# Optimization experiments

Hardware: AMD Instinct MI355X
Metric: run time of the kernel (lower is better)

## Reference

```python
import jax, jax.numpy as jnp
import numpy as np

B, T, E, H, D = 2, 2048, 1024, 16, 64
SCALE = 1.0 / float(np.sqrt(D))


def setup_inputs() -> dict:
    key = jax.random.key(0)
    ks = jax.random.split(key, 8)
    n = lambda k, sh, s=1.0: jax.random.normal(k, sh, dtype=jnp.float32) * s
    # torch nn.Linear weights are [out_features, in_features]; xavier-ish scale
    return {
        "query": n(ks[0], (B, T, E)),
        "key_": n(ks[1], (B, T, E)),
        "value": n(ks[2], (B, T, E)),
        "attn_mask": n(ks[3], (T, T), 0.1),
        "Wq": n(ks[4], (H * D, E), 1.0 / float(np.sqrt(E))),
        "Wk": n(ks[5], (H * D, E), 1.0 / float(np.sqrt(E))),
        "Wv": n(ks[6], (H * D, E), 1.0 / float(np.sqrt(E))),
        "Wo": n(ks[7], (E, H * D), 1.0 / float(np.sqrt(H * D))),
    }


def reference(query, key_, value, attn_mask, Wq, Wk, Wv, Wo):
    # projections (no bias), reshape to [B, T, H, D]
    Q = (query @ Wq.T).reshape(B, T, H, D)
    K = (key_ @ Wk.T).reshape(B, -1, H, D)
    V = (value @ Wv.T).reshape(B, -1, H, D)
    # scores [B, T, H, S]; additive [T, S] mask broadcast over B and H
    score = jnp.einsum("bthd,bshd->bths", Q, K) * SCALE
    score = score + attn_mask[:, None, :]
    prob = jax.nn.softmax(score, axis=-1)  # dropout is identity in eval mode
    attn = jnp.einsum("bths,bshd->bthd", prob, V)  # [B, T, H, D]
    x = attn.reshape(B, T, H * D) @ Wo.T  # output projection
    return x
```

## Files before the change

kernel.cpp:

```cpp
#include <hip/hip_runtime.h>


typedef __attribute__((ext_vector_type(8))) short s8v;
typedef __attribute__((ext_vector_type(4))) float f4v;

typedef __attribute__((address_space(1))) const void* gas_t;
typedef __attribute__((address_space(3))) void* las_t;

#define GLOAD_LDS(src, dst) \
  __builtin_amdgcn_global_load_lds((gas_t)(src), (las_t)(dst), 16, 0, 0)
#define MFMA16(a, b, c) __builtin_amdgcn_mfma_f32_16x16x32_bf16((a), (b), (c), 0, 0, 0)

#if __has_builtin(__builtin_amdgcn_exp2f)
#define EXP2(x) __builtin_amdgcn_exp2f(x)
#else
#define EXP2(x) exp2f(x)
#endif

static constexpr int Bn = 2, Tn = 2048, En = 1024, Hn = 16, Dn = 64;
static constexpr float kScale = 0.125f;
static constexpr float kLog2e = 1.4426950408889634f;

union P8 { s8v v; unsigned short u[8]; };

__device__ __forceinline__ unsigned short f2bf(float f) {
  unsigned int x = __float_as_uint(f);
  x += 0x7fffu + ((x >> 16) & 1u);
  return (unsigned short)(x >> 16);
}

__device__ __forceinline__ int cvtpk(float lo, float hi) {
  int r;
  asm("v_cvt_pk_bf16_f32 %0, %1, %2" : "=v"(r) : "v"(lo), "v"(hi));
  return r;
}

__device__ __forceinline__ void cast8(const float* __restrict__ src, int j,
                                      unsigned short* __restrict__ out, int i) {
  float4 a = ((const float4*)src)[2 * j];
  float4 b = ((const float4*)src)[2 * j + 1];
  P8 p;
  p.u[0] = f2bf(a.x); p.u[1] = f2bf(a.y); p.u[2] = f2bf(a.z); p.u[3] = f2bf(a.w);
  p.u[4] = f2bf(b.x); p.u[5] = f2bf(b.y); p.u[6] = f2bf(b.z); p.u[7] = f2bf(b.w);
  ((s8v*)out)[i] = p.v;
}

__global__ void cast3_kernel(const float* __restrict__ a, const float* __restrict__ b,
                             const float* __restrict__ c,
                             unsigned short* __restrict__ out, int n8) {
  int i = blockIdx.x * blockDim.x + threadIdx.x;
  const int stride = gridDim.x * blockDim.x;
  const int total = 3 * n8;
  for (; i < total; i += stride) {
    const float* src = (i < n8) ? a : (i < 2 * n8) ? b : c;
    const int j = (i < n8) ? i : (i < 2 * n8) ? i - n8 : i - 2 * n8;
    cast8(src, j, out, i);
  }
}

__global__ void cast4_kernel(const float* __restrict__ a, const float* __restrict__ b,
                             const float* __restrict__ c, const float* __restrict__ d,
                             unsigned short* __restrict__ out, int n8) {
  int i = blockIdx.x * blockDim.x + threadIdx.x;
  const int stride = gridDim.x * blockDim.x;
  const int total = 4 * n8;
  for (; i < total; i += stride) {
    const int which = i / n8;
    const float* src = (which == 0) ? a : (which == 1) ? b : (which == 2) ? c : d;
    cast8(src, i - which * n8, out, i);
  }
}

__global__ __launch_bounds__(64) void maskpack_kernel(const float* __restrict__ mask,
                                                      unsigned int* __restrict__ mPB) {
  __shared__ float tile[16][65];
  const int qt = blockIdx.x, st = blockIdx.y;
  const int tid = threadIdx.x;
#pragma unroll
  for (int i = 0; i < 16; ++i)
    tile[i][tid] = mask[(size_t)(qt * 16 + i) * Tn + st * 64 + tid];
  __syncthreads();
  const int lr = tid & 15, lg = tid >> 4;
  float o[16];
#pragma unroll
  for (int n = 0; n < 4; ++n)
#pragma unroll
    for (int rg = 0; rg < 4; ++rg)
      o[n * 4 + rg] = tile[lr][n * 16 + lg * 4 + rg] * kLog2e;
  unsigned int wds[8];
#pragma unroll
  for (int i = 0; i < 8; ++i)
    wds[i] = ((unsigned int)f2bf(o[2 * i + 1]) << 16) | f2bf(o[2 * i]);
  uint4* dst = (uint4*)(mPB + ((size_t)(qt * 32 + st) * 64 + tid) * 8);
  dst[0] = make_uint4(wds[0], wds[1], wds[2], wds[3]);
  dst[1] = make_uint4(wds[4], wds[5], wds[6], wds[7]);
}

__global__ __launch_bounds__(256) void gemm3_kernel(
    const unsigned short* __restrict__ qx, const unsigned short* __restrict__ kx,
    const unsigned short* __restrict__ vxa, const unsigned short* __restrict__ wqx,
    const unsigned short* __restrict__ wkx, const unsigned short* __restrict__ wvx,
    unsigned short* __restrict__ Qh, unsigned short* __restrict__ Kh,
    unsigned short* __restrict__ Vtg) {
  constexpr int K = 1024;
  __shared__ unsigned short As[128 * 64];
  __shared__ unsigned short Bs[128 * 64];
  const int tid = threadIdx.x;
  const int w = tid >> 6, l = tid & 63;
  const int wr = w >> 1, wc = w & 1;
  const int lr = l & 15, lg = l >> 4;

  const int id0 = blockIdx.x;
  const int rid = (id0 & 7) * 96 + (id0 >> 3);
  const int z = rid >> 8;
  const int t8 = rid & 255;
  const int m0 = (z < 2) ? (t8 >> 3) * 128 : (t8 & 7) * 128;
  const int n0 = (z < 2) ? (t8 & 7) * 128 : (t8 >> 3) * 128;

  const unsigned short* A = (z == 0) ? qx : (z == 1) ? kx : wvx;
  const unsigned short* W = (z == 0) ? wqx : (z == 1) ? wkx : vxa;

  f4v acc[4][4] = {};

  for (int k0 = 0; k0 < K; k0 += 64) {
#pragma unroll
    for (int jj = 0; jj < 4; ++jj) {
      const int q = jj * 256 + tid;
      const int r = q >> 3, c = q & 7;
      const int cs = c ^ (r & 7);
      GLOAD_LDS(A + (size_t)(m0 + r) * K + k0 + cs * 8,
                (char*)As + (jj * 256 + w * 64) * 16);
      GLOAD_LDS(W + (size_t)(n0 + r) * K + k0 + cs * 8,
                (char*)Bs + (jj * 256 + w * 64) * 16);
    }
    __syncthreads();
#pragma unroll
    for (int kk = 0; kk < 2; ++kk) {
      s8v af[4], bf[4];
      const int kc = kk * 4 + lg;
#pragma unroll
      for (int i = 0; i < 4; ++i) {
        const int ra = wr * 64 + i * 16 + lr;
        const int rb = wc * 64 + i * 16 + lr;
        af[i] = *(const s8v*)((const char*)As + ra * 128 + ((kc ^ (ra & 7)) << 4));
        bf[i] = *(const s8v*)((const char*)Bs + rb * 128 + ((kc ^ (rb & 7)) << 4));
      }
#pragma unroll
      for (int mi = 0; mi < 4; ++mi)
#pragma unroll
        for (int nj = 0; nj < 4; ++nj)
          acc[mi][nj] = MFMA16(af[mi], bf[nj], acc[mi][nj]);
    }
    __syncthreads();
  }

  const float scale = (z == 0) ? kScale * kLog2e : 1.0f;
#pragma unroll
  for (int mi = 0; mi < 4; ++mi)
#pragma unroll
    for (int nj = 0; nj < 4; ++nj)
#pragma unroll
      for (int rg = 0; rg < 4; ++rg) {
        const int row = m0 + wr * 64 + mi * 16 + lg * 4 + rg;
        const int col = n0 + wc * 64 + nj * 16 + lr;
        const float v = acc[mi][nj][rg];
        if (z < 2) {
          const int b = row >> 11, t = row & (Tn - 1);
          const int hh = col >> 6, d = col & 63;
          unsigned short* o = (z == 0) ? Qh : Kh;
          o[(((size_t)(b * Hn + hh) * Tn + t) << 6) + d] = f2bf(v * scale);
        } else {
          const int hh = row >> 6, d = row & 63;
          const int b = col >> 11, t = col & (Tn - 1);
          Vtg[((size_t)(b * Hn + hh) * 64 + d) * Tn + t] = f2bf(v);
        }
      }
}

__global__ __launch_bounds__(256) void gemm_out(const unsigned short* __restrict__ A,
                                                const unsigned short* __restrict__ W,
                                                float* __restrict__ Cout) {
  constexpr int N = 1024, K = 1024;
  __shared__ unsigned short As[2][128 * 64];
  __shared__ unsigned short Bs[2][128 * 64];
  const int tid = threadIdx.x;
  const int w = tid >> 6, l = tid & 63;
  const int wr = w >> 1, wc = w & 1;
  const int lr = l & 15, lg = l >> 4;

  const int gx = gridDim.x;
  int id = blockIdx.y * gx + blockIdx.x;
  id = (id & 7) * 32 + (id >> 3);
  const int m0 = (id / gx) * 128, n0 = (id % gx) * 128;

  auto stage = [&](int k0, int buf) {
#pragma unroll
    for (int jj = 0; jj < 4; ++jj) {
      const int q = jj * 256 + tid;
      const int r = q >> 3, c = q & 7;
      const int cs = c ^ (r & 7);
      GLOAD_LDS(A + (size_t)(m0 + r) * K + k0 + cs * 8,
                (char*)As[buf] + (jj * 256 + w * 64) * 16);
      GLOAD_LDS(W + (size_t)(n0 + r) * K + k0 + cs * 8,
                (char*)Bs[buf] + (jj * 256 + w * 64) * 16);
    }
  };

  stage(0, 0);
  __syncthreads();

  f4v acc[4][4] = {};

  for (int k0 = 0, t = 0; k0 < K; k0 += 64, ++t) {
    const int cur = t & 1;
    if (k0 + 64 < K) stage(k0 + 64, cur ^ 1);
#pragma unroll
    for (int kk = 0; kk < 2; ++kk) {
      s8v af[4], bf[4];
      const int kc = kk * 4 + lg;
#pragma unroll
      for (int i = 0; i < 4; ++i) {
        const int ra = wr * 64 + i * 16 + lr;
        const int rb = wc * 64 + i * 16 + lr;
        af[i] = *(const s8v*)((const char*)As[cur] + ra * 128 + ((kc ^ (ra & 7)) << 4));
        bf[i] = *(const s8v*)((const char*)Bs[cur] + rb * 128 + ((kc ^ (rb & 7)) << 4));
      }
#pragma unroll
      for (int mi = 0; mi < 4; ++mi)
#pragma unroll
        for (int nj = 0; nj < 4; ++nj)
          acc[mi][nj] = MFMA16(af[mi], bf[nj], acc[mi][nj]);
    }
    __syncthreads();
  }

#pragma unroll
  for (int mi = 0; mi < 4; ++mi)
#pragma unroll
    for (int nj = 0; nj < 4; ++nj)
#pragma unroll
      for (int rg = 0; rg < 4; ++rg) {
        const int row = m0 + wr * 64 + mi * 16 + lg * 4 + rg;
        const int col = n0 + wc * 64 + nj * 16 + lr;
        Cout[(size_t)row * N + col] = acc[mi][nj][rg];
      }
}

__global__ __launch_bounds__(128, 2) void attn_kernel(
    const unsigned short* __restrict__ Q,
    const unsigned short* __restrict__ Kg,
    const unsigned short* __restrict__ Vt,
    const unsigned int* __restrict__ mPB,
    unsigned short* __restrict__ Out) {
  __shared__ unsigned short Ks[2][64 * 64];
  __shared__ unsigned short Vs[2][64 * 64];

  const int tid = threadIdx.x;
  const int w = tid >> 6, lane = tid & 63;
  const int lr = lane & 15, lg = lane >> 4;

  const int lin = blockIdx.x;
  const int xcd = lin & 7, slot = lin >> 3;
  const int bh = xcd * 4 + (slot >> 5);
  const int qtB = slot & 31;
  const int b = bh >> 4, h = bh & 15;

  const size_t hoff = (size_t)bh * Tn * Dn;
  const unsigned short* Qh = Q + hoff;
  const unsigned short* Kh = Kg + hoff;
  const unsigned short* Vh = Vt + hoff;
  const int qwA = qtB * 64 + w * 32;
  const int qwB = qwA + 16;
  const unsigned int* mp = mPB + ((size_t)(qtB * 4 + w * 2) * 2048 + lane) * 8;

  auto stage = [&](int s0, int buf) {
#pragma unroll
    for (int jj = 0; jj < 4; ++jj) {
      const int cq = jj * 128 + tid;
      const int r = cq >> 3, cc = cq & 7;
      const int cs = cc ^ (r & 7);
      GLOAD_LDS(Kh + (size_t)(s0 + r) * 64 + cs * 8,
                (char*)Ks[buf] + (jj * 128 + w * 64) * 16);
      GLOAD_LDS(Vh + (size_t)r * Tn + s0 + cs * 8,
                (char*)Vs[buf] + (jj * 128 + w * 64) * 16);
    }
  };

  s8v qfA[2], qfB[2];
#pragma unroll
  for (int kk = 0; kk < 2; ++kk) {
    qfA[kk] = *(const s8v*)(Qh + (size_t)(qwA + lr) * 64 + kk * 32 + lg * 8);
    qfB[kk] = *(const s8v*)(Qh + (size_t)(qwB + lr) * 64 + kk * 32 + lg * 8);
  }

  float lsumA = 0.f, lsumB = 0.f;
  f4v oaccA[4] = {}, oaccB[4] = {};

  const int srcA = lr + ((lg & 1) << 5);
  const int srcB = srcA + 16;
  const int hi = lg >> 1;

  stage(0, 0);
  __syncthreads();

  for (int s0 = 0, t = 0; s0 < Tn; s0 += 64, ++t, mp += 512) {
    const int cur = t & 1;
    if (s0 + 64 < Tn) stage(s0 + 64, cur ^ 1);

    s8v kf[2][4], vf[2][4];
#pragma unroll
    for (int kk = 0; kk < 2; ++kk)
#pragma unroll
      for (int n = 0; n < 4; ++n) {
        const int row = n * 16 + lr;
        const int coff = ((kk * 4 + lg) ^ (lr & 7)) << 4;
        kf[kk][n] = *(const s8v*)((const char*)Ks[cur] + row * 128 + coff);
        vf[kk][n] = *(const s8v*)((const char*)Vs[cur] + row * 128 + coff);
      }

    {
      const uint4 u0 = *(const uint4*)(mp);
      const uint4 u1 = *(const uint4*)(mp + 4);
      const unsigned int wd[8] = {u0.x, u0.y, u0.z, u0.w, u1.x, u1.y, u1.z, u1.w};
      f4v scT[4];
#pragma unroll
      for (int n = 0; n < 4; ++n) {
        scT[n][0] = __uint_as_float(wd[2 * n] << 16);
        scT[n][1] = __uint_as_float(wd[2 * n] & 0xffff0000u);
        scT[n][2] = __uint_as_float(wd[2 * n + 1] << 16);
        scT[n][3] = __uint_as_float(wd[2 * n + 1] & 0xffff0000u);
      }
#pragma unroll
      for (int kk = 0; kk < 2; ++kk)
#pragma unroll
        for (int n = 0; n < 4; ++n)
          scT[n] = MFMA16(kf[kk][n], qfA[kk], scT[n]);
      float ssum = 0.f;
#pragma unroll
      for (int n = 0; n < 4; ++n)
#pragma unroll
        for (int rg = 0; rg < 4; ++rg) {
          const float p = EXP2(scT[n][rg]);
          scT[n][rg] = p;
          ssum += p;
        }
      ssum += __shfl_xor(ssum, 16);
      ssum += __shfl_xor(ssum, 32);
      lsumA += ssum;
      int pw0[4], pw1[4];
#pragma unroll
      for (int n = 0; n < 4; ++n) {
        pw0[n] = cvtpk(scT[n][0], scT[n][1]);
        pw1[n] = cvtpk(scT[n][2], scT[n][3]);
      }
#pragma unroll
      for (int kk = 0; kk < 2; ++kk) {
        const int a0 = __shfl(pw0[2 * kk], srcA), b0 = __shfl(pw0[2 * kk + 1], srcA);
        const int a1 = __shfl(pw1[2 * kk], srcA), b1 = __shfl(pw1[2 * kk + 1], srcA);
        const int a2 = __shfl(pw0[2 * kk], srcB), b2 = __shfl(pw0[2 * kk + 1], srcB);
        const int a3 = __shfl(pw1[2 * kk], srcB), b3 = __shfl(pw1[2 * kk + 1], srcB);
        union { s8v v; int x[4]; } pf;
        pf.x[0] = hi ? b0 : a0;
        pf.x[1] = hi ? b1 : a1;
        pf.x[2] = hi ? b2 : a2;
        pf.x[3] = hi ? b3 : a3;
#pragma unroll
        for (int n = 0; n < 4; ++n)
          oaccA[n] = MFMA16(pf.v, vf[kk][n], oaccA[n]);
      }
    }

    {
      const uint4 u0 = *(const uint4*)(mp + 16384);
      const uint4 u1 = *(const uint4*)(mp + 16388);
      const unsigned int wd[8] = {u0.x, u0.y, u0.z, u0.w, u1.x, u1.y, u1.z, u1.w};
      f4v scT[4];
#pragma unroll
      for (int n = 0; n < 4; ++n) {
        scT[n][0] = __uint_as_float(wd[2 * n] << 16);
        scT[n][1] = __uint_as_float(wd[2 * n] & 0xffff0000u);
        scT[n][2] = __uint_as_float(wd[2 * n + 1] << 16);
        scT[n][3] = __uint_as_float(wd[2 * n + 1] & 0xffff0000u);
      }
#pragma unroll
      for (int kk = 0; kk < 2; ++kk)
#pragma unroll
        for (int n = 0; n < 4; ++n)
          scT[n] = MFMA16(kf[kk][n], qfB[kk], scT[n]);
      float ssum = 0.f;
#pragma unroll
      for (int n = 0; n < 4; ++n)
#pragma unroll
        for (int rg = 0; rg < 4; ++rg) {
          const float p = EXP2(scT[n][rg]);
          scT[n][rg] = p;
          ssum += p;
        }
      ssum += __shfl_xor(ssum, 16);
      ssum += __shfl_xor(ssum, 32);
      lsumB += ssum;
      int pw0[4], pw1[4];
#pragma unroll
      for (int n = 0; n < 4; ++n) {
        pw0[n] = cvtpk(scT[n][0], scT[n][1]);
        pw1[n] = cvtpk(scT[n][2], scT[n][3]);
      }
#pragma unroll
      for (int kk = 0; kk < 2; ++kk) {
        const int a0 = __shfl(pw0[2 * kk], srcA), b0 = __shfl(pw0[2 * kk + 1], srcA);
        const int a1 = __shfl(pw1[2 * kk], srcA), b1 = __shfl(pw1[2 * kk + 1], srcA);
        const int a2 = __shfl(pw0[2 * kk], srcB), b2 = __shfl(pw0[2 * kk + 1], srcB);
        const int a3 = __shfl(pw1[2 * kk], srcB), b3 = __shfl(pw1[2 * kk + 1], srcB);
        union { s8v v; int x[4]; } pf;
        pf.x[0] = hi ? b0 : a0;
        pf.x[1] = hi ? b1 : a1;
        pf.x[2] = hi ? b2 : a2;
        pf.x[3] = hi ? b3 : a3;
#pragma unroll
        for (int n = 0; n < 4; ++n)
          oaccB[n] = MFMA16(pf.v, vf[kk][n], oaccB[n]);
      }
    }

    __syncthreads();
  }

#pragma unroll
  for (int rg = 0; rg < 4; ++rg) {
    const float invA = 1.f / __shfl(lsumA, lg * 4 + rg);
    const float invB = 1.f / __shfl(lsumB, lg * 4 + rg);
    const int tA = qwA + lg * 4 + rg;
    const int tB = qwB + lg * 4 + rg;
#pragma unroll
    for (int n = 0; n < 4; ++n) {
      const int d = n * 16 + lr;
      Out[((size_t)(b * Tn + tA) * Hn + h) * 64 + d] = f2bf(oaccA[n][rg] * invA);
      Out[((size_t)(b * Tn + tB) * Hn + h) * 64 + d] = f2bf(oaccB[n][rg] * invB);
    }
  }
}

extern "C" void kernel_launch(void* const* d_in, const int* in_sizes, int n_in,
                              void* d_out, int out_size, void* d_ws, size_t ws_size,
                              hipStream_t stream) {
  (void)in_sizes; (void)n_in; (void)out_size; (void)ws_size;
  const float* query = (const float*)d_in[0];
  const float* key_  = (const float*)d_in[1];
  const float* value = (const float*)d_in[2];
  const float* mask  = (const float*)d_in[3];
  const float* Wq    = (const float*)d_in[4];
  const float* Wk    = (const float*)d_in[5];
  const float* Wv    = (const float*)d_in[6];
  const float* Wo    = (const float*)d_in[7];
  float* out = (float*)d_out;

  char* ws = (char*)d_ws;
  const size_t MB = 1024 * 1024;
  unsigned short* qx  = (unsigned short*)(ws + 0 * MB);
  unsigned short* kx  = (unsigned short*)(ws + 8 * MB);
  unsigned short* vx  = (unsigned short*)(ws + 16 * MB);
  unsigned short* Qh  = (unsigned short*)(ws + 24 * MB);
  unsigned short* Kh  = (unsigned short*)(ws + 32 * MB);
  unsigned short* Vtg = (unsigned short*)(ws + 40 * MB);
  unsigned short* atb = (unsigned short*)(ws + 48 * MB);
  unsigned short* wqx = (unsigned short*)(ws + 56 * MB);
  unsigned short* wkx = (unsigned short*)(ws + 58 * MB);
  unsigned short* wvx = (unsigned short*)(ws + 60 * MB);
  unsigned short* wox = (unsigned short*)(ws + 62 * MB);
  unsigned int* mPB = (unsigned int*)(ws + 0 * MB);

  const int nBig = Bn * Tn * En / 8;
  const int nW   = En * En / 8;
  cast3_kernel<<<2048, 256, 0, stream>>>(query, key_, value, qx, nBig);
  cast4_kernel<<<1024, 256, 0, stream>>>(Wq, Wk, Wv, Wo, wqx, nW);

  gemm3_kernel<<<768, 256, 0, stream>>>(qx, kx, vx, wqx, wkx, wvx, Qh, Kh, Vtg);

  maskpack_kernel<<<dim3(128, 32), 64, 0, stream>>>(mask, mPB);

  attn_kernel<<<1024, 128, 0, stream>>>(Qh, Kh, Vtg, mPB, atb);

  gemm_out<<<dim3(8, 32), 256, 0, stream>>>(atb, wox, out);
}
```

Measured before the change: 166.2 us.

## Split attention over two KV halves and merge partials in a combine kernel

The attention kernel now launches twice as many blocks, and each block handles half of the key/value sequence. Each block writes unnormalized fp16 partial outputs and per-row softmax sums. A new combine kernel adds the two partials, divides by the summed denominators and writes the bf16 attention output. The aim is more parallelism and better latency hiding on the CUs. In exchange it adds an extra kernel launch, more memory traffic for the partials, and fp16 range risk on unnormalized accumulators. The workspace is reused by aliasing buffers that are no longer needed.

```diff
diff --git a/kernel.cpp b/kernel.cpp
--- a/kernel.cpp
+++ b/kernel.cpp
@@ -27,6 +27,12 @@
   unsigned int x = __float_as_uint(f);
   x += 0x7fffu + ((x >> 16) & 1u);
   return (unsigned short)(x >> 16);
+}
+
+__device__ __forceinline__ unsigned short f2h(float f) {
+  union { _Float16 h; unsigned short u; } c;
+  c.h = (_Float16)f;
+  return c.u;
 }
 
 __device__ __forceinline__ int cvtpk(float lo, float hi) {
@@ -251,7 +257,8 @@
     const unsigned short* __restrict__ Kg,
     const unsigned short* __restrict__ Vt,
     const unsigned int* __restrict__ mPB,
-    unsigned short* __restrict__ Out) {
+    unsigned short* __restrict__ oP0, unsigned short* __restrict__ oP1,
+    float* __restrict__ ls0, float* __restrict__ ls1) {
   __shared__ unsigned short Ks[2][64 * 64];
   __shared__ unsigned short Vs[2][64 * 64];
 
@@ -260,7 +267,9 @@
   const int lr = lane & 15, lg = lane >> 4;
 
   const int lin = blockIdx.x;
-  const int xcd = lin & 7, slot = lin >> 3;
+  const int half = lin >> 10;
+  const int l10 = lin & 1023;
+  const int xcd = l10 & 7, slot = l10 >> 3;
   const int bh = xcd * 4 + (slot >> 5);
   const int qtB = slot & 31;
   const int b = bh >> 4, h = bh & 15;
@@ -271,7 +280,12 @@
   const unsigned short* Vh = Vt + hoff;
   const int qwA = qtB * 64 + w * 32;
   const int qwB = qwA + 16;
-  const unsigned int* mp = mPB + ((size_t)(qtB * 4 + w * 2) * 2048 + lane) * 8;
+  const unsigned int* mp =
+      mPB + ((size_t)(qtB * 4 + w * 2) * 2048 + lane) * 8 + half * 8192;
+  const int sBeg = half * 1024, sEnd = sBeg + 1024;
+
+  unsigned short* oph = half ? oP1 : oP0;
+  float* lsh = half ? ls1 : ls0;
 
   auto stage = [&](int s0, int buf) {
 #pragma unroll
@@ -300,12 +314,12 @@
   const int srcB = srcA + 16;
   const int hi = lg >> 1;
 
-  stage(0, 0);
+  stage(sBeg, 0);
   __syncthreads();
 
-  for (int s0 = 0, t = 0; s0 < Tn; s0 += 64, ++t, mp += 512) {
+  for (int s0 = sBeg, t = 0; s0 < sEnd; s0 += 64, ++t, mp += 512) {
     const int cur = t & 1;
-    if (s0 + 64 < Tn) stage(s0 + 64, cur ^ 1);
+    if (s0 + 64 < sEnd) stage(s0 + 64, cur ^ 1);
 
     s8v kf[2][4], vf[2][4];
 #pragma unroll
@@ -427,17 +441,37 @@
 
 #pragma unroll
   for (int rg = 0; rg < 4; ++rg) {
-    const float invA = 1.f / __shfl(lsumA, lg * 4 + rg);
-    const float invB = 1.f / __shfl(lsumB, lg * 4 + rg);
     const int tA = qwA + lg * 4 + rg;
     const int tB = qwB + lg * 4 + rg;
 #pragma unroll
     for (int n = 0; n < 4; ++n) {
       const int d = n * 16 + lr;
-      Out[((size_t)(b * Tn + tA) * Hn + h) * 64 + d] = f2bf(oaccA[n][rg] * invA);
-      Out[((size_t)(b * Tn + tB) * Hn + h) * 64 + d] = f2bf(oaccB[n][rg] * invB);
-    }
-  }
+      oph[((size_t)(b * Tn + tA) * Hn + h) * 64 + d] = f2h(oaccA[n][rg]);
+      oph[((size_t)(b * Tn + tB) * Hn + h) * 64 + d] = f2h(oaccB[n][rg]);
+    }
+  }
+  if (lg == 0) {
+    lsh[(size_t)(b * Tn + qwA + lr) * Hn + h] = lsumA;
+    lsh[(size_t)(b * Tn + qwB + lr) * Hn + h] = lsumB;
+  }
+}
+
+__global__ __launch_bounds__(256) void combine_kernel(
+    const unsigned short* __restrict__ oP0, const unsigned short* __restrict__ oP1,
+    const float* __restrict__ ls0, const float* __restrict__ ls1,
+    unsigned short* __restrict__ atb) {
+  const int idx = blockIdx.x * 256 + threadIdx.x;
+  const int row = idx >> 3;
+  const size_t base = (size_t)idx * 8;
+  union H8 { s8v v; _Float16 h[8]; } a, c;
+  a.v = *(const s8v*)(oP0 + base);
+  c.v = *(const s8v*)(oP1 + base);
+  const float inv = 1.f / (ls0[row] + ls1[row]);
+  P8 p;
+#pragma unroll
+  for (int j = 0; j < 8; ++j)
+    p.u[j] = f2bf(((float)a.h[j] + (float)c.h[j]) * inv);
+  *(s8v*)(atb + base) = p.v;
 }
 
 extern "C" void kernel_launch(void* const* d_in, const int* in_sizes, int n_in,
@@ -462,12 +496,16 @@
   unsigned short* Qh  = (unsigned short*)(ws + 24 * MB);
   unsigned short* Kh  = (unsigned short*)(ws + 32 * MB);
   unsigned short* Vtg = (unsigned short*)(ws + 40 * MB);
-  unsigned short* atb = (unsigned short*)(ws + 48 * MB);
+  unsigned short* oP1 = (unsigned short*)(ws + 48 * MB);
   unsigned short* wqx = (unsigned short*)(ws + 56 * MB);
   unsigned short* wkx = (unsigned short*)(ws + 58 * MB);
   unsigned short* wvx = (unsigned short*)(ws + 60 * MB);
   unsigned short* wox = (unsigned short*)(ws + 62 * MB);
-  unsigned int* mPB = (unsigned int*)(ws + 0 * MB);
+  unsigned int*   mPB = (unsigned int*)(ws + 0 * MB);
+  unsigned short* oP0 = (unsigned short*)(ws + 9 * MB);
+  float* ls0 = (float*)(ws + 17 * MB);
+  float* ls1 = (float*)(ws + 17 * MB + 256 * 1024);
+  unsigned short* atb = Qh;
 
   const int nBig = Bn * Tn * En / 8;
   const int nW   = En * En / 8;
@@ -478,7 +516,9 @@
 
   maskpack_kernel<<<dim3(128, 32), 64, 0, stream>>>(mask, mPB);
 
-  attn_kernel<<<1024, 128, 0, stream>>>(Qh, Kh, Vtg, mPB, atb);
+  attn_kernel<<<2048, 128, 0, stream>>>(Qh, Kh, Vtg, mPB, oP0, oP1, ls0, ls1);
+
+  combine_kernel<<<2048, 256, 0, stream>>>(oP0, oP1, ls0, ls1, atb);
 
   gemm_out<<<dim3(8, 32), 256, 0, stream>>>(atb, wox, out);
 }
```

After: 169.5 us. About the same (+2.0%).
